# Optimization experiments

Hardware: AMD Instinct MI355X
Metric: run time of the kernel (lower is better)

The kernel has to match this reference:

```python
import jax, jax.numpy as jnp
import numpy as np

EPS = 1e-5
NUM_HEADS = 16

def layernorm(x, g, b):
    mu = jnp.mean(x, axis=-1, keepdims=True)
    var = jnp.mean(jnp.square(x - mu), axis=-1, keepdims=True)
    return (x - mu) * jax.lax.rsqrt(var + EPS) * g + b

def setup_inputs() -> dict:
    key = jax.random.key(0)
    ks = jax.random.split(key, 5)
    B, N, C = 2, 2048, 1024
    s_in = 1.0 / np.sqrt(C)
    return {
        "x": jax.random.normal(ks[0], (B, N, C), jnp.float32),
        "ln1_g": jnp.ones((C,), jnp.float32),
        "ln1_b": jnp.zeros((C,), jnp.float32),
        "w_qk": jax.random.normal(ks[1], (C, 2 * C), jnp.float32) * s_in,
        "w_v": jax.random.normal(ks[2], (C, C), jnp.float32) * s_in,
        "ln2_g": jnp.ones((C,), jnp.float32),
        "ln2_b": jnp.zeros((C,), jnp.float32),
        "w_proj": jax.random.normal(ks[3], (C, C), jnp.float32) * s_in,
        "b_proj": jnp.zeros((C,), jnp.float32),
    }

def reference(x, ln1_g, ln1_b, w_qk, w_v, ln2_g, ln2_b, w_proj, b_proj):
    B, N, C = x.shape
    H = NUM_HEADS
    hd = C // H
    scale = hd ** (-0.5)
    xn = layernorm(x, ln1_g, ln1_b)
    # qk: [B,N,2C] -> q,k each [B,H,N,hd]
    qk = (xn @ w_qk).reshape(B, N, 2, H, hd).transpose(2, 0, 3, 1, 4)
    q, k = qk[0], qk[1]
    v = (xn @ w_v).reshape(B, N, H, hd).transpose(0, 2, 1, 3)  # [B,H,N,hd]
    attn = jnp.einsum("bhqd,bhkd->bhqk", q, k) * scale
    attn = jax.nn.softmax(attn, axis=-1)
    out = jnp.einsum("bhqk,bhkd->bhqd", attn, v)  # [B,H,N,hd]
    out = out.transpose(0, 2, 1, 3).reshape(B, N, C)
    out = layernorm(out, ln2_g, ln2_b)
    return out @ w_proj + b_proj
```

## Files before the change

kernel.cpp:

```cpp
#include <hip/hip_runtime.h>
#include <hip/hip_bf16.h>


typedef __attribute__((ext_vector_type(8))) short short8;
typedef __attribute__((ext_vector_type(4))) short short4v;
typedef __attribute__((ext_vector_type(4))) float float4v;
typedef __attribute__((ext_vector_type(4))) unsigned uint4v;

__device__ __forceinline__ unsigned short f2bf(float f) {
    unsigned u = __builtin_bit_cast(unsigned, f);
    return (unsigned short)((u + 0x7FFFu + ((u >> 16) & 1u)) >> 16);
}
__device__ __forceinline__ unsigned cvtpk(float lo, float hi) {
    unsigned r;
    asm("v_cvt_pk_bf16_f32 %0, %1, %2" : "=v"(r) : "v"(lo), "v"(hi));
    return r;
}
__device__ __forceinline__ void gll16(const unsigned short* g, unsigned short* l) {
    __builtin_amdgcn_global_load_lds(
        (const __attribute__((address_space(1))) unsigned int*)g,
        (__attribute__((address_space(3))) unsigned int*)l, 16, 0, 0);
}

__global__ __launch_bounds__(256) void prep(
    const float* __restrict__ x, const float* __restrict__ g1, const float* __restrict__ b1,
    const float* __restrict__ w_qk, const float* __restrict__ w_v,
    const float* __restrict__ w_proj, const float* __restrict__ g2,
    const float* __restrict__ b2,
    unsigned short* __restrict__ xn, unsigned short* __restrict__ wqkvT,
    unsigned short* __restrict__ wgT, float* __restrict__ u, float* __restrict__ w0) {
    __shared__ float sh[64 * 65];
    const int bid = blockIdx.x, tid = threadIdx.x;
    if (bid < 1024) {
        const int lane = tid & 63;
        const int row = bid * 4 + (tid >> 6);
        const float4* xr = reinterpret_cast<const float4*>(x + (size_t)row * 1024);
        const float4* G4 = reinterpret_cast<const float4*>(g1);
        const float4* B4 = reinterpret_cast<const float4*>(b1);
        float4 v[4];
        float s = 0.f, sq = 0.f;
#pragma unroll
        for (int i = 0; i < 4; i++) {
            v[i] = xr[i * 64 + lane];
            s  += (v[i].x + v[i].y) + (v[i].z + v[i].w);
            sq += (v[i].x * v[i].x + v[i].y * v[i].y) + (v[i].z * v[i].z + v[i].w * v[i].w);
        }
#pragma unroll
        for (int off = 32; off >= 1; off >>= 1) {
            s  += __shfl_xor(s, off, 64);
            sq += __shfl_xor(sq, off, 64);
        }
        const float mu = s * (1.f / 1024.f);
        const float rstd = rsqrtf(sq * (1.f / 1024.f) - mu * mu + 1e-5f);
#pragma unroll
        for (int i = 0; i < 4; i++) {
            const float4 gv = G4[i * 64 + lane], bv = B4[i * 64 + lane];
            ushort4 o;
            o.x = f2bf((v[i].x - mu) * rstd * gv.x + bv.x);
            o.y = f2bf((v[i].y - mu) * rstd * gv.y + bv.y);
            o.z = f2bf((v[i].z - mu) * rstd * gv.z + bv.z);
            o.w = f2bf((v[i].w - mu) * rstd * gv.w + bv.w);
            *reinterpret_cast<ushort4*>(&xn[(size_t)row * 1024 + i * 256 + lane * 4]) = o;
        }
    } else {
        const float* in; unsigned short* out; int Cc, bx, by; bool doU = false;
        if (bid < 1536)      { int t = bid - 1024; in = w_qk;   out = wqkvT;               Cc = 2048; bx = t & 31; by = t >> 5; }
        else if (bid < 1792) { int t = bid - 1536; in = w_v;    out = wqkvT + 2048 * 1024; Cc = 1024; bx = t & 15; by = t >> 4; }
        else                 { int t = bid - 1792; in = w_proj; out = wgT; doU = true;     Cc = 1024; bx = t & 15; by = t >> 4; }
        const int c0 = bx * 64, r0 = by * 64;
        const int tx16 = tid & 15, ty = tid >> 4;
#pragma unroll
        for (int i = 0; i < 4; i++) {
            const float4 rv = *reinterpret_cast<const float4*>(
                &in[(size_t)(r0 + i * 16 + ty) * Cc + c0 + tx16 * 4]);
            float* d = &sh[(i * 16 + ty) * 65 + tx16 * 4];
            d[0] = rv.x; d[1] = rv.y; d[2] = rv.z; d[3] = rv.w;
        }
        __syncthreads();
        float4 gv = {1.f, 1.f, 1.f, 1.f}, bv = {0.f, 0.f, 0.f, 0.f};
        if (doU) {
            gv = *reinterpret_cast<const float4*>(&g2[r0 + tx16 * 4]);
            bv = *reinterpret_cast<const float4*>(&b2[r0 + tx16 * 4]);
        }
#pragma unroll
        for (int i = 0; i < 4; i++) {
            const int lc = i * 16 + ty;
            const float a0 = sh[(tx16 * 4 + 0) * 65 + lc];
            const float a1 = sh[(tx16 * 4 + 1) * 65 + lc];
            const float a2 = sh[(tx16 * 4 + 2) * 65 + lc];
            const float a3 = sh[(tx16 * 4 + 3) * 65 + lc];
            const float s0 = a0 * gv.x, s1 = a1 * gv.y, s2 = a2 * gv.z, s3 = a3 * gv.w;
            const ushort4 st = {f2bf(s0), f2bf(s1), f2bf(s2), f2bf(s3)};
            *reinterpret_cast<ushort4*>(
                &out[(size_t)(c0 + lc) * 1024 + r0 + tx16 * 4]) = st;
            if (doU) {
                float pu = (s0 + s1) + (s2 + s3);
                float pw = (a0 * bv.x + a1 * bv.y) + (a2 * bv.z + a3 * bv.w);
#pragma unroll
                for (int off = 1; off <= 8; off <<= 1) {
                    pu += __shfl_xor(pu, off, 64);
                    pw += __shfl_xor(pw, off, 64);
                }
                if (tx16 == 0) {
                    atomicAdd(&u[c0 + lc], pu);
                    atomicAdd(&w0[c0 + lc], pw);
                }
            }
        }
    }
}

__global__ __launch_bounds__(512, 2) void gemm_qkv(const unsigned short* __restrict__ A,
                                                   const unsigned short* __restrict__ Bt,
                                                   unsigned short* __restrict__ qb,
                                                   unsigned short* __restrict__ kb,
                                                   unsigned short* __restrict__ vT) {
    __shared__ unsigned short As[2 * 128 * 64];
    __shared__ unsigned short Bs[2 * 192 * 64];
    const int tid = threadIdx.x, lane = tid & 63, w = tid >> 6;
    const int wm = (w >> 2) * 64, wn = (w & 3) * 48;
    const int quad = lane >> 4, l16 = lane & 15;
    const int ls = lane >> 3, sg = lane & 7;
    const int m0 = blockIdx.y * 128, n0 = blockIdx.x * 192;

    float4v acc[4][3];
#pragma unroll
    for (int mi = 0; mi < 4; mi++)
#pragma unroll
        for (int ni = 0; ni < 3; ni++) acc[mi][ni] = float4v{0.f, 0.f, 0.f, 0.f};

    const int g = (sg ^ ls) * 8;
#pragma unroll
    for (int i = 0; i < 2; i++)
        gll16(&A[(size_t)(m0 + w * 16 + i * 8 + ls) * 1024 + g], &As[(w * 16 + i * 8) * 64]);
#pragma unroll
    for (int i = 0; i < 3; i++)
        gll16(&Bt[(size_t)(n0 + w * 24 + i * 8 + ls) * 1024 + g], &Bs[(w * 24 + i * 8) * 64]);

#pragma unroll 1
    for (int s = 0; s < 16; s++) {
        __syncthreads();
        if (s + 1 < 16) {
            const int k0 = (s + 1) << 6;
            unsigned short* Ad = As + (((s + 1) & 1) << 13);
            unsigned short* Bd = Bs + (((s + 1) & 1) * 12288);
#pragma unroll
            for (int i = 0; i < 2; i++)
                gll16(&A[(size_t)(m0 + w * 16 + i * 8 + ls) * 1024 + k0 + g],
                      &Ad[(w * 16 + i * 8) * 64]);
#pragma unroll
            for (int i = 0; i < 3; i++)
                gll16(&Bt[(size_t)(n0 + w * 24 + i * 8 + ls) * 1024 + k0 + g],
                      &Bd[(w * 24 + i * 8) * 64]);
        }
        const unsigned short* Ac = As + ((s & 1) << 13);
        const unsigned short* Bc = Bs + ((s & 1) * 12288);
#pragma unroll
        for (int ks = 0; ks < 2; ks++) {
            short8 af[4], bfr[3];
#pragma unroll
            for (int mi = 0; mi < 4; mi++) {
                const int r = wm + mi * 16 + l16;
                af[mi] = *reinterpret_cast<const short8*>(
                    &Ac[r * 64 + ((ks * 4 + quad) ^ (r & 7)) * 8]);
            }
#pragma unroll
            for (int ni = 0; ni < 3; ni++) {
                const int r = wn + ni * 16 + l16;
                bfr[ni] = *reinterpret_cast<const short8*>(
                    &Bc[r * 64 + ((ks * 4 + quad) ^ (r & 7)) * 8]);
            }
#pragma unroll
            for (int mi = 0; mi < 4; mi++)
#pragma unroll
                for (int ni = 0; ni < 3; ni++)
                    acc[mi][ni] = __builtin_amdgcn_mfma_f32_16x16x32_bf16(
                        af[mi], bfr[ni], acc[mi][ni], 0, 0, 0);
        }
    }

    const float QSCALE = 0.125f * 1.4426950408889634f;
#pragma unroll
    for (int mi = 0; mi < 4; mi++) {
        const int row0 = m0 + wm + mi * 16 + quad * 4;
        const int b = row0 >> 11, nq = row0 & 2047;
#pragma unroll
        for (int ni = 0; ni < 3; ni++) {
            const int col = n0 + wn + ni * 16 + l16;
            if (col < 1024) {
                const int h = col >> 6, d = col & 63;
#pragma unroll
                for (int r = 0; r < 4; r++)
                    qb[(((size_t)b * 16 + h) * 2048 + nq + r) * 64 + d] =
                        f2bf(acc[mi][ni][r] * QSCALE);
            } else if (col < 2048) {
                const int c = col - 1024, h = c >> 6, d = c & 63;
#pragma unroll
                for (int r = 0; r < 4; r++)
                    kb[(((size_t)b * 16 + h) * 2048 + nq + r) * 64 + d] = f2bf(acc[mi][ni][r]);
            } else {
                const int c = col - 2048, h = c >> 6, d = c & 63;
                const short4v sv = {(short)f2bf(acc[mi][ni][0]), (short)f2bf(acc[mi][ni][1]),
                                    (short)f2bf(acc[mi][ni][2]), (short)f2bf(acc[mi][ni][3])};
                *reinterpret_cast<short4v*>(
                    &vT[(((size_t)b * 16 + h) * 64 + d) * 2048 + nq]) = sv;
            }
        }
    }
}

__global__ __launch_bounds__(512, 4) void flash_attn(const unsigned short* __restrict__ qbuf,
                                                     const unsigned short* __restrict__ kb,
                                                     const unsigned short* __restrict__ vT,
                                                     unsigned short* __restrict__ attn,
                                                     float2* __restrict__ part) {
    __shared__ __align__(16) unsigned short KB[2][2][64 * 64];
    __shared__ __align__(16) unsigned short VB[2][2][64 * 64];
    __shared__ float lsh[4][2][64];
    const int tid = threadIdx.x, lane = tid & 63, w = tid >> 6;
    const int wq = w & 3, kh = w >> 2;
    const int quad = lane >> 4, l16 = lane & 15;
    const int ls = lane >> 3, sg = lane & 7;
    const int bh = blockIdx.x, q0 = blockIdx.y * 128;
    const size_t nbase = (size_t)bh * 2048;

    const int pr = w * 8 + ls;
    const int srow = (pr & 32) | ((pr & 12) << 1) | ((pr & 16) >> 2) | (pr & 3);
    const int sgran = (sg ^ ls) << 3;

    short8 bq[2][2];
#pragma unroll
    for (int q2 = 0; q2 < 2; q2++)
#pragma unroll
        for (int ks = 0; ks < 2; ks++)
            bq[q2][ks] = *reinterpret_cast<const short8*>(
                &qbuf[(nbase + q0 + wq * 32 + q2 * 16 + l16) * 64 + ks * 32 + quad * 8]);

    float l_part[2] = {0.f, 0.f};
    float4v o_acc[2][4];
#pragma unroll
    for (int q2 = 0; q2 < 2; q2++)
#pragma unroll
        for (int db = 0; db < 4; db++) o_acc[q2][db] = float4v{0.f, 0.f, 0.f, 0.f};

#define FSTAGE(t, buf)                                                                  \
    _Pragma("unroll")                                                                   \
    for (int t2 = 0; t2 < 2; t2++) {                                                    \
        gll16(&kb[(nbase + (t) * 128 + t2 * 64 + srow) * 64 + sgran],                   \
              &KB[buf][t2][w * 8 * 64]);                                                \
        gll16(&vT[((size_t)bh * 64 + w * 8 + ls) * 2048 + (t) * 128 + t2 * 64 + sgran], \
              &VB[buf][t2][w * 8 * 64]);                                                \
    }

    FSTAGE(0, 0);

#pragma unroll 1
    for (int s = 0; s < 16; s++) {
        __syncthreads();
        if (s + 1 < 16) FSTAGE(s + 1, (s + 1) & 1);

#pragma unroll
        for (int t2 = 0; t2 < 2; t2++) {
            const unsigned short* Kc = KB[s & 1][t2];
            const unsigned short* Vc = VB[s & 1][t2];

            short8 kf[2][2];
#pragma unroll
            for (int ks = 0; ks < 2; ks++)
#pragma unroll
                for (int cc = 0; cc < 2; cc++) {
                    const int r = kh * 32 + cc * 16 + l16;
                    kf[ks][cc] = *reinterpret_cast<const short8*>(
                        &Kc[r * 64 + ((ks * 4 + quad) ^ (r & 7)) * 8]);
                }
            short8 va[4];
#pragma unroll
            for (int db = 0; db < 4; db++) {
                const int r = db * 16 + l16;
                va[db] = *reinterpret_cast<const short8*>(
                    &Vc[r * 64 + ((kh * 4 + quad) ^ (r & 7)) * 8]);
            }

#pragma unroll
            for (int q2 = 0; q2 < 2; q2++) {
                float4v s_acc[2];
#pragma unroll
                for (int cc = 0; cc < 2; cc++) s_acc[cc] = float4v{0.f, 0.f, 0.f, 0.f};
                __builtin_amdgcn_s_setprio(1);
#pragma unroll
                for (int ks = 0; ks < 2; ks++)
#pragma unroll
                    for (int cc = 0; cc < 2; cc++)
                        s_acc[cc] = __builtin_amdgcn_mfma_f32_16x16x32_bf16(
                            kf[ks][cc], bq[q2][ks], s_acc[cc], 0, 0, 0);
                __builtin_amdgcn_s_setprio(0);

                float ls2 = 0.f;
                float p[8];
#pragma unroll
                for (int cc = 0; cc < 2; cc++)
#pragma unroll
                    for (int r = 0; r < 4; r++) {
                        const float pv = __builtin_amdgcn_exp2f(s_acc[cc][r]);
                        p[cc * 4 + r] = pv;
                        ls2 += pv;
                    }
                uint4v pd;
                pd.x = cvtpk(p[0], p[1]); pd.y = cvtpk(p[2], p[3]);
                pd.z = cvtpk(p[4], p[5]); pd.w = cvtpk(p[6], p[7]);
                const short8 pb = __builtin_bit_cast(short8, pd);
                l_part[q2] += ls2;
                __builtin_amdgcn_s_setprio(1);
#pragma unroll
                for (int db = 0; db < 4; db++)
                    o_acc[q2][db] = __builtin_amdgcn_mfma_f32_16x16x32_bf16(
                        va[db], pb, o_acc[q2][db], 0, 0, 0);
                __builtin_amdgcn_s_setprio(0);
            }
        }
    }
#undef FSTAGE

    __syncthreads();
    float* osh = reinterpret_cast<float*>(KB);
    const int swz = (l16 & 7) << 2;
    if (kh == 1) {
#pragma unroll
        for (int q2 = 0; q2 < 2; q2++) {
#pragma unroll
            for (int db = 0; db < 4; db++) {
                const int base = (wq * 32 + q2 * 16 + l16) * 64 + db * 16 + quad * 4;
                *reinterpret_cast<float4v*>(&osh[base ^ swz]) = o_acc[q2][db];
            }
            lsh[wq][q2][lane] = l_part[q2];
        }
    }
    __syncthreads();
    if (kh == 0) {
        const int b = bh >> 4, h = bh & 15;
#pragma unroll
        for (int q2 = 0; q2 < 2; q2++) {
            float lr = l_part[q2] + lsh[wq][q2][lane];
            lr += __shfl_xor(lr, 16, 64);
            lr += __shfl_xor(lr, 32, 64);
            const float inv = 1.f / lr;
            const int grow = b * 2048 + q0 + wq * 32 + q2 * 16 + l16;
            float sum = 0.f, s2 = 0.f;
#pragma unroll
            for (int db = 0; db < 4; db++) {
                const int base = (wq * 32 + q2 * 16 + l16) * 64 + db * 16 + quad * 4;
                const float4v oh = *reinterpret_cast<const float4v*>(&osh[base ^ swz]);
                const float o0 = (o_acc[q2][db][0] + oh[0]) * inv;
                const float o1 = (o_acc[q2][db][1] + oh[1]) * inv;
                const float o2 = (o_acc[q2][db][2] + oh[2]) * inv;
                const float o3 = (o_acc[q2][db][3] + oh[3]) * inv;
                const ushort4 st = {f2bf(o0), f2bf(o1), f2bf(o2), f2bf(o3)};
                *reinterpret_cast<ushort4*>(
                    &attn[(size_t)grow * 1024 + h * 64 + db * 16 + quad * 4]) = st;
                sum += (o0 + o1) + (o2 + o3);
                s2  += (o0 * o0 + o1 * o1) + (o2 * o2 + o3 * o3);
            }
            sum += __shfl_xor(sum, 16, 64); sum += __shfl_xor(sum, 32, 64);
            s2  += __shfl_xor(s2, 16, 64);  s2  += __shfl_xor(s2, 32, 64);
            if (quad == 0) part[(size_t)grow * 16 + h] = float2{sum, s2};
        }
    }
}

__global__ __launch_bounds__(256) void gemm_proj(const unsigned short* __restrict__ A,
                                                 const unsigned short* __restrict__ Bt,
                                                 const float2* __restrict__ part,
                                                 const float* __restrict__ u,
                                                 const float* __restrict__ w0,
                                                 const float* __restrict__ bias,
                                                 float* __restrict__ out) {
    __shared__ unsigned short As[2 * 64 * 64];
    __shared__ unsigned short Bs[2 * 64 * 64];
    __shared__ float2 rstat_s[64];
    const int tid = threadIdx.x, lane = tid & 63, w = tid >> 6;
    const int wm = (w >> 1) * 32, wn = (w & 1) * 32;
    const int quad = lane >> 4, l16 = lane & 15;
    const int ls = lane >> 3, sg = lane & 7;
    const int m0 = blockIdx.y * 64, n0 = blockIdx.x * 64;
    {
        const int rloc = tid >> 2, qtr = tid & 3;
        const float4* p4 = reinterpret_cast<const float4*>(part);
        float s = 0.f, s2 = 0.f;
#pragma unroll
        for (int j = 0; j < 2; j++) {
            const float4 p = p4[(size_t)(m0 + rloc) * 8 + qtr * 2 + j];
            s += p.x + p.z; s2 += p.y + p.w;
        }
        s  += __shfl_xor(s, 1, 64);  s  += __shfl_xor(s, 2, 64);
        s2 += __shfl_xor(s2, 1, 64); s2 += __shfl_xor(s2, 2, 64);
        if (!qtr) {
            const float mu = s * (1.f / 1024.f);
            const float rstd = rsqrtf(s2 * (1.f / 1024.f) - mu * mu + 1e-5f);
            rstat_s[rloc] = float2{rstd, mu * rstd};
        }
    }

    float4v acc[2][2];
#pragma unroll
    for (int mi = 0; mi < 2; mi++)
#pragma unroll
        for (int ni = 0; ni < 2; ni++) acc[mi][ni] = float4v{0.f, 0.f, 0.f, 0.f};

    const int g = (sg ^ ls) * 8;
#pragma unroll
    for (int i = 0; i < 2; i++) {
        gll16(&A[(size_t)(m0 + w * 16 + i * 8 + ls) * 1024 + g], &As[(w * 16 + i * 8) * 64]);
        gll16(&Bt[(size_t)(n0 + w * 16 + i * 8 + ls) * 1024 + g], &Bs[(w * 16 + i * 8) * 64]);
    }

#pragma unroll 1
    for (int s = 0; s < 16; s++) {
        __syncthreads();
        if (s + 1 < 16) {
            const int k0 = (s + 1) << 6;
            unsigned short* Ad = As + (((s + 1) & 1) << 12);
            unsigned short* Bd = Bs + (((s + 1) & 1) << 12);
#pragma unroll
            for (int i = 0; i < 2; i++) {
                gll16(&A[(size_t)(m0 + w * 16 + i * 8 + ls) * 1024 + k0 + g],
                      &Ad[(w * 16 + i * 8) * 64]);
                gll16(&Bt[(size_t)(n0 + w * 16 + i * 8 + ls) * 1024 + k0 + g],
                      &Bd[(w * 16 + i * 8) * 64]);
            }
        }
        const unsigned short* Ac = As + ((s & 1) << 12);
        const unsigned short* Bc = Bs + ((s & 1) << 12);
#pragma unroll
        for (int ks = 0; ks < 2; ks++) {
            short8 af[2], bfr[2];
#pragma unroll
            for (int mi = 0; mi < 2; mi++) {
                const int r = wm + mi * 16 + l16;
                af[mi] = *reinterpret_cast<const short8*>(
                    &Ac[r * 64 + ((ks * 4 + quad) ^ (r & 7)) * 8]);
            }
#pragma unroll
            for (int ni = 0; ni < 2; ni++) {
                const int r = wn + ni * 16 + l16;
                bfr[ni] = *reinterpret_cast<const short8*>(
                    &Bc[r * 64 + ((ks * 4 + quad) ^ (r & 7)) * 8]);
            }
#pragma unroll
            for (int mi = 0; mi < 2; mi++)
#pragma unroll
                for (int ni = 0; ni < 2; ni++)
                    acc[mi][ni] = __builtin_amdgcn_mfma_f32_16x16x32_bf16(
                        af[mi], bfr[ni], acc[mi][ni], 0, 0, 0);
        }
    }

#pragma unroll
    for (int mi = 0; mi < 2; mi++) {
        const int rl0 = wm + mi * 16 + quad * 4;
        float2 rs[4];
#pragma unroll
        for (int r = 0; r < 4; r++) rs[r] = rstat_s[rl0 + r];
#pragma unroll
        for (int ni = 0; ni < 2; ni++) {
            const int col = n0 + wn + ni * 16 + l16;
            const float uu = u[col], ww = w0[col] + bias[col];
#pragma unroll
            for (int r = 0; r < 4; r++)
                out[(size_t)(m0 + rl0 + r) * 1024 + col] =
                    fmaf(rs[r].x, acc[mi][ni][r], ww - rs[r].y * uu);
        }
    }
}

extern "C" void kernel_launch(void* const* d_in, const int* in_sizes, int n_in,
                              void* d_out, int out_size, void* d_ws, size_t ws_size,
                              hipStream_t stream) {
    const float* x      = (const float*)d_in[0];
    const float* ln1_g  = (const float*)d_in[1];
    const float* ln1_b  = (const float*)d_in[2];
    const float* w_qk   = (const float*)d_in[3];
    const float* w_v    = (const float*)d_in[4];
    const float* ln2_g  = (const float*)d_in[5];
    const float* ln2_b  = (const float*)d_in[6];
    const float* w_proj = (const float*)d_in[7];
    const float* b_proj = (const float*)d_in[8];
    float* out = (float*)d_out;

    char* ws = (char*)d_ws;
    unsigned short* xn      = (unsigned short*)(ws + 0);
    unsigned short* wqkvT   = (unsigned short*)(ws + 8388608);
    unsigned short* wgT     = (unsigned short*)(ws + 14680064);
    unsigned short* qbuf    = (unsigned short*)(ws + 16777216);
    unsigned short* kbuf    = (unsigned short*)(ws + 25165824);
    unsigned short* vTbuf   = (unsigned short*)(ws + 33554432);
    unsigned short* attn    = (unsigned short*)(ws + 41943040);
    float2*         part    = (float2*)(ws + 50331648);
    float*          u       = (float*)(ws + 50888704);
    float*          w0      = (float*)(ws + 50892800);

    hipMemsetAsync(ws + 50888704, 0, 8192, stream);
    prep<<<2048, 256, 0, stream>>>(x, ln1_g, ln1_b, w_qk, w_v, w_proj, ln2_g, ln2_b,
                                   xn, wqkvT, wgT, u, w0);
    gemm_qkv<<<dim3(16, 32), 512, 0, stream>>>(xn, wqkvT, qbuf, kbuf, vTbuf);
    flash_attn<<<dim3(32, 16), 512, 0, stream>>>(qbuf, kbuf, vTbuf, attn, part);
    gemm_proj<<<dim3(16, 64), 256, 0, stream>>>(attn, wgT, part, u, w0, b_proj, out);
}
```

Before: 185.9 us.

## Load K/V fragments directly from global memory instead of staging through LDS

```diff
diff --git a/kernel.cpp b/kernel.cpp
--- a/kernel.cpp
+++ b/kernel.cpp
@@ -214,19 +214,30 @@
                                                      const unsigned short* __restrict__ vT,
                                                      unsigned short* __restrict__ attn,
                                                      float2* __restrict__ part) {
-    __shared__ __align__(16) unsigned short KB[2][2][64 * 64];
-    __shared__ __align__(16) unsigned short VB[2][2][64 * 64];
+    __shared__ __align__(16) float osh[128 * 64];
     __shared__ float lsh[4][2][64];
     const int tid = threadIdx.x, lane = tid & 63, w = tid >> 6;
     const int wq = w & 3, kh = w >> 2;
     const int quad = lane >> 4, l16 = lane & 15;
-    const int ls = lane >> 3, sg = lane & 7;
     const int bh = blockIdx.x, q0 = blockIdx.y * 128;
     const size_t nbase = (size_t)bh * 2048;
 
-    const int pr = w * 8 + ls;
-    const int srow = (pr & 32) | ((pr & 12) << 1) | ((pr & 16) >> 2) | (pr & 3);
-    const int sgran = (sg ^ ls) << 3;
+    int ka[2];
+#pragma unroll
+    for (int cc = 0; cc < 2; cc++) {
+        const int p = kh * 32 + cc * 16 + l16;
+        ka[cc] = (p & 32) | ((p & 12) << 1) | ((p & 16) >> 2) | (p & 3);
+    }
+    const unsigned short* kp[2][2];
+#pragma unroll
+    for (int ks = 0; ks < 2; ks++)
+#pragma unroll
+        for (int cc = 0; cc < 2; cc++)
+            kp[ks][cc] = &kb[(nbase + ka[cc]) * 64 + ks * 32 + quad * 8];
+    const unsigned short* vp[4];
+#pragma unroll
+    for (int db = 0; db < 4; db++)
+        vp[db] = &vT[((size_t)bh * 64 + db * 16 + l16) * 2048 + kh * 32 + quad * 8];
 
     short8 bq[2][2];
 #pragma unroll
@@ -243,86 +254,57 @@
 #pragma unroll
         for (int db = 0; db < 4; db++) o_acc[q2][db] = float4v{0.f, 0.f, 0.f, 0.f};
 
-#define FSTAGE(t, buf)                                                                  \
-    _Pragma("unroll")                                                                   \
-    for (int t2 = 0; t2 < 2; t2++) {                                                    \
-        gll16(&kb[(nbase + (t) * 128 + t2 * 64 + srow) * 64 + sgran],                   \
-              &KB[buf][t2][w * 8 * 64]);                                                \
-        gll16(&vT[((size_t)bh * 64 + w * 8 + ls) * 2048 + (t) * 128 + t2 * 64 + sgran], \
-              &VB[buf][t2][w * 8 * 64]);                                                \
-    }
-
-    FSTAGE(0, 0);
-
 #pragma unroll 1
-    for (int s = 0; s < 16; s++) {
-        __syncthreads();
-        if (s + 1 < 16) FSTAGE(s + 1, (s + 1) & 1);
-
-#pragma unroll
-        for (int t2 = 0; t2 < 2; t2++) {
-            const unsigned short* Kc = KB[s & 1][t2];
-            const unsigned short* Vc = VB[s & 1][t2];
-
-            short8 kf[2][2];
+    for (int s = 0; s < 32; s++) {
+        short8 kf[2][2], va[4];
+#pragma unroll
+        for (int ks = 0; ks < 2; ks++)
+#pragma unroll
+            for (int cc = 0; cc < 2; cc++)
+                kf[ks][cc] = *reinterpret_cast<const short8*>(kp[ks][cc] + (size_t)s * 4096);
+#pragma unroll
+        for (int db = 0; db < 4; db++)
+            va[db] = *reinterpret_cast<const short8*>(vp[db] + s * 64);
+
+#pragma unroll
+        for (int q2 = 0; q2 < 2; q2++) {
+            float4v s_acc[2];
+#pragma unroll
+            for (int cc = 0; cc < 2; cc++) s_acc[cc] = float4v{0.f, 0.f, 0.f, 0.f};
+            __builtin_amdgcn_s_setprio(1);
 #pragma unroll
             for (int ks = 0; ks < 2; ks++)
 #pragma unroll
-                for (int cc = 0; cc < 2; cc++) {
-                    const int r = kh * 32 + cc * 16 + l16;
-                    kf[ks][cc] = *reinterpret_cast<const short8*>(
-                        &Kc[r * 64 + ((ks * 4 + quad) ^ (r & 7)) * 8]);
+                for (int cc = 0; cc < 2; cc++)
+                    s_acc[cc] = __builtin_amdgcn_mfma_f32_16x16x32_bf16(
+                        kf[ks][cc], bq[q2][ks], s_acc[cc], 0, 0, 0);
+            __builtin_amdgcn_s_setprio(0);
+
+            float ls2 = 0.f;
+            float p[8];
+#pragma unroll
+            for (int cc = 0; cc < 2; cc++)
+#pragma unroll
+                for (int r = 0; r < 4; r++) {
+                    const float pv = __builtin_amdgcn_exp2f(s_acc[cc][r]);
+                    p[cc * 4 + r] = pv;
+                    ls2 += pv;
                 }
-            short8 va[4];
-#pragma unroll
-            for (int db = 0; db < 4; db++) {
-                const int r = db * 16 + l16;
-                va[db] = *reinterpret_cast<const short8*>(
-                    &Vc[r * 64 + ((kh * 4 + quad) ^ (r & 7)) * 8]);
-            }
-
-#pragma unroll
-            for (int q2 = 0; q2 < 2; q2++) {
-                float4v s_acc[2];
-#pragma unroll
-                for (int cc = 0; cc < 2; cc++) s_acc[cc] = float4v{0.f, 0.f, 0.f, 0.f};
-                __builtin_amdgcn_s_setprio(1);
-#pragma unroll
-                for (int ks = 0; ks < 2; ks++)
-#pragma unroll
-                    for (int cc = 0; cc < 2; cc++)
-                        s_acc[cc] = __builtin_amdgcn_mfma_f32_16x16x32_bf16(
-                            kf[ks][cc], bq[q2][ks], s_acc[cc], 0, 0, 0);
-                __builtin_amdgcn_s_setprio(0);
-
-                float ls2 = 0.f;
-                float p[8];
-#pragma unroll
-                for (int cc = 0; cc < 2; cc++)
-#pragma unroll
-                    for (int r = 0; r < 4; r++) {
-                        const float pv = __builtin_amdgcn_exp2f(s_acc[cc][r]);
-                        p[cc * 4 + r] = pv;
-                        ls2 += pv;
-                    }
-                uint4v pd;
-                pd.x = cvtpk(p[0], p[1]); pd.y = cvtpk(p[2], p[3]);
-                pd.z = cvtpk(p[4], p[5]); pd.w = cvtpk(p[6], p[7]);
-                const short8 pb = __builtin_bit_cast(short8, pd);
-                l_part[q2] += ls2;
-                __builtin_amdgcn_s_setprio(1);
-#pragma unroll
-                for (int db = 0; db < 4; db++)
-                    o_acc[q2][db] = __builtin_amdgcn_mfma_f32_16x16x32_bf16(
-                        va[db], pb, o_acc[q2][db], 0, 0, 0);
-                __builtin_amdgcn_s_setprio(0);
-            }
-        }
-    }
-#undef FSTAGE
+            uint4v pd;
+            pd.x = cvtpk(p[0], p[1]); pd.y = cvtpk(p[2], p[3]);
+            pd.z = cvtpk(p[4], p[5]); pd.w = cvtpk(p[6], p[7]);
+            const short8 pb = __builtin_bit_cast(short8, pd);
+            l_part[q2] += ls2;
+            __builtin_amdgcn_s_setprio(1);
+#pragma unroll
+            for (int db = 0; db < 4; db++)
+                o_acc[q2][db] = __builtin_amdgcn_mfma_f32_16x16x32_bf16(
+                    va[db], pb, o_acc[q2][db], 0, 0, 0);
+            __builtin_amdgcn_s_setprio(0);
+        }
+    }
 
     __syncthreads();
-    float* osh = reinterpret_cast<float*>(KB);
     const int swz = (l16 & 7) << 2;
     if (kh == 1) {
 #pragma unroll
```

New measurement: 256.2 us. +37.8%, slower.
